# Optimization experiments

Measured on AMD Instinct MI355X. Metric: run time of the kernel, lower is better.

Reference implementation:

```python
import jax, jax.numpy as jnp
import numpy as np

D_MODEL, HEAD, B, S = 1024, 64, 4, 2048

def setup_inputs() -> dict:
    key = jax.random.key(0)
    ks = jax.random.split(key, 7)
    sc = 0.02
    return {
        "x": jax.random.normal(ks[0], (B, S, D_MODEL), dtype=jnp.float32),
        "w_q": jax.random.normal(ks[1], (D_MODEL, HEAD), dtype=jnp.float32) * sc,
        "b_q": jax.random.normal(ks[2], (HEAD,), dtype=jnp.float32) * sc,
        "w_k": jax.random.normal(ks[3], (D_MODEL, HEAD), dtype=jnp.float32) * sc,
        "b_k": jax.random.normal(ks[4], (HEAD,), dtype=jnp.float32) * sc,
        "w_v": jax.random.normal(ks[5], (D_MODEL, HEAD), dtype=jnp.float32) * sc,
        "b_v": jax.random.normal(ks[6], (HEAD,), dtype=jnp.float32) * sc,
    }

def reference(x, w_q, b_q, w_k, b_k, w_v, b_v):
    # q, k, v: [B, S, H]
    q = jnp.einsum('bsd,dh->bsh', x, w_q) + b_q
    k = jnp.einsum('bsd,dh->bsh', x, w_k) + b_k
    v = jnp.einsum('bsd,dh->bsh', x, w_v) + b_v
    head = k.shape[-1]
    # Source divides by (1/sqrt(d)) i.e. multiplies by sqrt(d) -- kept faithful.
    scores = jnp.einsum('bqh,bkh->bqk', q, k) * jnp.sqrt(jnp.float32(head))
    seq = x.shape[1]
    causal = jnp.tril(jnp.ones((seq, seq), dtype=bool))  # [S, S]
    scores = jnp.where(causal, scores, -jnp.inf)
    att = jax.nn.softmax(scores, axis=-1)
    # dropout is identity in eval / p=0
    return jnp.einsum('bqk,bkh->bqh', att, v)
```

## Files before the change

### kernel.cpp

```cpp
#include <hip/hip_runtime.h>
#include <math.h>

#define D_MODEL 1024
#define HEAD 64
#define BATCH 4
#define SEQ 2048
#define M_TOT (BATCH*SEQ)

typedef short short8 __attribute__((ext_vector_type(8)));
typedef float f32x4 __attribute__((ext_vector_type(4)));
typedef unsigned short ushort_t;

__device__ __forceinline__ unsigned short f2bf(float x) {
    union { float f; unsigned u; } v; v.f = x;
    unsigned r = (v.u + 0x7FFFu + ((v.u >> 16) & 1u)) >> 16;
    return (unsigned short)r;
}
__device__ __forceinline__ unsigned short f2bf_trunc(float x) {
    union { float f; unsigned u; } v; v.f = x;
    return (unsigned short)(v.u >> 16);
}
__device__ __forceinline__ float bf2f(unsigned short h) {
    union { unsigned u; float f; } v; v.u = ((unsigned)h) << 16;
    return v.f;
}

__global__ __launch_bounds__(256) void wsplit_kernel(
    const float* __restrict__ wq, const float* __restrict__ wk,
    const float* __restrict__ wv,
    ushort_t* __restrict__ Wfhi, ushort_t* __restrict__ Wflo)
{
    int tid = blockIdx.x * 256 + threadIdx.x;
    int l = tid & 63;
    int c = l & 15, g = l >> 4;
    int rest = tid >> 6;
    int nt = rest % 12, ks = rest / 12;
    const float* W = (nt < 4) ? wq : ((nt < 8) ? wk : wv);
    int colm = ((nt & 3) * 16) + c;
    short8 hi, lo;
#pragma unroll
    for (int e = 0; e < 8; ++e) {
        float v = W[(size_t)(32 * ks + 8 * g + e) * HEAD + colm];
        unsigned short h = f2bf_trunc(v);
        hi[e] = (short)h;
        lo[e] = (short)f2bf(v - bf2f(h));
    }
    *(short8*)&Wfhi[(size_t)tid * 8] = hi;
    *(short8*)&Wflo[(size_t)tid * 8] = lo;
}

__global__ __launch_bounds__(256) void proj_kernel(
    const float* __restrict__ x,
    const ushort_t* __restrict__ Wfhi, const ushort_t* __restrict__ Wflo,
    const float* __restrict__ bq, const float* __restrict__ bk,
    const float* __restrict__ bv,
    ushort_t* __restrict__ Qhi, ushort_t* __restrict__ Qlo,
    ushort_t* __restrict__ Khi, ushort_t* __restrict__ Klo,
    ushort_t* __restrict__ Vt)
{
    __shared__ float ld[4][16][33];
    const int t = threadIdx.x;
    const int w = t >> 6;
    const int l = t & 63;
    const int c = l & 15, g = l >> 4;
    const int job = blockIdx.x * 4 + w;
    const int mt = job / 6;
    const int ntg = job - mt * 6;
    const int m0 = mt * 16;

    f32x4 acc0 = (f32x4)0.0f, acc1 = (f32x4)0.0f;

    const float* xrow = &x[(size_t)(m0 + c) * D_MODEL + 8 * g];
    const size_t wbase = (size_t)(ntg * 2) * 512 + (size_t)l * 8;

#pragma unroll 4
    for (int ks = 0; ks < 32; ++ks) {
        const float* xp = xrow + 32 * ks;
        float4 a = *(const float4*)xp;
        float4 b2 = *(const float4*)(xp + 4);
        float xs[8] = {a.x, a.y, a.z, a.w, b2.x, b2.y, b2.z, b2.w};
        short8 xh, xl;
#pragma unroll
        for (int e = 0; e < 8; ++e) {
            unsigned short h = f2bf_trunc(xs[e]);
            xh[e] = (short)h;
            xl[e] = (short)f2bf(xs[e] - bf2f(h));
        }
        const size_t wo = wbase + (size_t)ks * 6144;
        short8 wh0 = *(const short8*)&Wfhi[wo];
        short8 wl0 = *(const short8*)&Wflo[wo];
        short8 wh1 = *(const short8*)&Wfhi[wo + 512];
        short8 wl1 = *(const short8*)&Wflo[wo + 512];
        acc0 = __builtin_amdgcn_mfma_f32_16x16x32_bf16(xh, wh0, acc0, 0, 0, 0);
        acc1 = __builtin_amdgcn_mfma_f32_16x16x32_bf16(xh, wh1, acc1, 0, 0, 0);
        acc0 = __builtin_amdgcn_mfma_f32_16x16x32_bf16(xl, wh0, acc0, 0, 0, 0);
        acc1 = __builtin_amdgcn_mfma_f32_16x16x32_bf16(xl, wh1, acc1, 0, 0, 0);
        acc0 = __builtin_amdgcn_mfma_f32_16x16x32_bf16(xh, wl0, acc0, 0, 0, 0);
        acc1 = __builtin_amdgcn_mfma_f32_16x16x32_bf16(xh, wl1, acc1, 0, 0, 0);
    }

#pragma unroll
    for (int r = 0; r < 4; ++r) {
        ld[w][4 * g + r][c] = acc0[r];
        ld[w][4 * g + r][16 + c] = acc1[r];
    }

    const int b = m0 >> 11;
    const int s0 = m0 & 2047;
    const int cb32 = (ntg & 1) * 32;

    if (ntg < 4) {
        const int row = l >> 2, cc = (l & 3) * 8;
        const float* bias = (ntg < 2) ? bq : bk;
        const float scale = (ntg < 2) ? 8.0f : 1.0f;
        ushort_t* Dhi = (ntg < 2) ? Qhi : Khi;
        ushort_t* Dlo = (ntg < 2) ? Qlo : Klo;
        short8 hi, lo;
#pragma unroll
        for (int i = 0; i < 8; ++i) {
            float v = (ld[w][row][cc + i] + bias[cb32 + cc + i]) * scale;
            unsigned short h = f2bf_trunc(v);
            hi[i] = (short)h;
            lo[i] = (short)f2bf(v - bf2f(h));
        }
        *(short8*)&Dhi[(size_t)(m0 + row) * HEAD + cb32 + cc] = hi;
        *(short8*)&Dlo[(size_t)(m0 + row) * HEAD + cb32 + cc] = lo;
    } else {
        const int dl = l >> 1, sh = (l & 1) * 8;
        const float bb = bv[cb32 + dl];
        short8 vv;
#pragma unroll
        for (int i = 0; i < 8; ++i)
            vv[i] = (short)f2bf(ld[w][sh + i][dl] + bb);
        *(short8*)&Vt[((size_t)b * HEAD + cb32 + dl) * SEQ + s0 + sh] = vv;
    }
}

#define NW 4
#define CHUNK 16

__global__ __launch_bounds__(256) void attn_kernel(
    const ushort_t* __restrict__ Qhi, const ushort_t* __restrict__ Qlo,
    const ushort_t* __restrict__ Khi, const ushort_t* __restrict__ Klo,
    const ushort_t* __restrict__ Vt, float* __restrict__ out)
{
    __shared__ float Po[NW][CHUNK][68];
    __shared__ float Pm[NW][CHUNK];
    __shared__ float Pl[NW][CHUNK];
    __shared__ __align__(16) ushort_t Plds[NW][CHUNK][72];

    const int t = threadIdx.x;
    const int w = t >> 6;
    const int l = t & 63;
    const int b = blockIdx.y;
    const int chunk = (int)gridDim.x - 1 - (int)blockIdx.x;
    const int q0 = chunk * CHUNK;
    const int c = l & 15;
    const int g = l >> 4;

    short8 qhi[2], qlo[2];
    {
        const ushort_t* qbase = &Qhi[(size_t)(b * SEQ + q0 + c) * HEAD];
        const ushort_t* qbasel = &Qlo[(size_t)(b * SEQ + q0 + c) * HEAD];
#pragma unroll
        for (int dc = 0; dc < 2; ++dc) {
            qhi[dc] = *(const short8*)&qbase[dc * 32 + 8 * g];
            qlo[dc] = *(const short8*)&qbasel[dc * 32 + 8 * g];
        }
    }

    f32x4 acc[4];
#pragma unroll
    for (int dt = 0; dt < 4; ++dt) acc[dt] = (f32x4)0.0f;
    float mrun = -1e30f, lsum = 0.f;

    const int ntiles = (q0 + CHUNK + 63) >> 6;
#pragma unroll 1
    for (int tile = w; tile < ntiles; tile += NW) {
        const int c0 = tile * 64;
        int nlive = ((q0 + 15 - c0) >> 4) + 1;
        nlive = nlive > 4 ? 4 : nlive;

        float sc[4][4];
        float pv[4][4];
#pragma unroll
        for (int t4 = 0; t4 < 4; ++t4)
#pragma unroll
            for (int r = 0; r < 4; ++r) pv[t4][r] = 0.f;

        float tmax = -1e30f;
#pragma unroll
        for (int t4 = 0; t4 < 4; ++t4) {
            if (t4 < nlive) {
                f32x4 st = (f32x4)0.0f;
                const size_t krow = (size_t)(b * SEQ + c0 + 16 * t4 + c) * HEAD;
#pragma unroll
                for (int dc = 0; dc < 2; ++dc) {
                    short8 khi = *(const short8*)&Khi[krow + dc * 32 + 8 * g];
                    short8 klo = *(const short8*)&Klo[krow + dc * 32 + 8 * g];
                    st = __builtin_amdgcn_mfma_f32_16x16x32_bf16(khi, qhi[dc], st, 0, 0, 0);
                    st = __builtin_amdgcn_mfma_f32_16x16x32_bf16(khi, qlo[dc], st, 0, 0, 0);
                    st = __builtin_amdgcn_mfma_f32_16x16x32_bf16(klo, qhi[dc], st, 0, 0, 0);
                }
#pragma unroll
                for (int r = 0; r < 4; ++r) {
                    int kv = c0 + 16 * t4 + 4 * g + r;
                    float s = (kv <= q0 + c) ? st[r] : -1e30f;
                    sc[t4][r] = s;
                    tmax = fmaxf(tmax, s);
                }
            }
        }
        tmax = fmaxf(tmax, __shfl_xor(tmax, 16));
        tmax = fmaxf(tmax, __shfl_xor(tmax, 32));
        float newm = fmaxf(mrun, tmax);
        float corr = __expf(mrun - newm);
        mrun = newm;

        float psum = 0.f;
#pragma unroll
        for (int t4 = 0; t4 < 4; ++t4) {
            if (t4 < nlive) {
#pragma unroll
                for (int r = 0; r < 4; ++r) {
                    float pp = __expf(sc[t4][r] - newm);
                    pv[t4][r] = pp;
                    psum += pp;
                }
            }
        }
        psum += __shfl_xor(psum, 16);
        psum += __shfl_xor(psum, 32);
        lsum = lsum * corr + psum;

#pragma unroll
        for (int r = 0; r < 4; ++r) {
            float cq = __shfl(corr, 4 * g + r);
#pragma unroll
            for (int dt = 0; dt < 4; ++dt) acc[dt][r] *= cq;
        }

#pragma unroll
        for (int t4 = 0; t4 < 4; ++t4) {
            uint2 u;
            u.x = (unsigned)f2bf(pv[t4][0]) | ((unsigned)f2bf(pv[t4][1]) << 16);
            u.y = (unsigned)f2bf(pv[t4][2]) | ((unsigned)f2bf(pv[t4][3]) << 16);
            *(uint2*)&Plds[w][c][16 * t4 + 4 * g] = u;
        }

        const int nkvc = (nlive + 1) >> 1;
#pragma unroll
        for (int kvc = 0; kvc < 2; ++kvc) {
            if (kvc < nkvc) {
                short8 pf = *(short8*)&Plds[w][c][kvc * 32 + 8 * g];
#pragma unroll
                for (int dt = 0; dt < 4; ++dt) {
                    const ushort_t* vp =
                        &Vt[((size_t)(b * HEAD) + 16 * dt + c) * SEQ + c0 + kvc * 32 + 8 * g];
                    short8 vf = *(const short8*)vp;
                    acc[dt] = __builtin_amdgcn_mfma_f32_16x16x32_bf16(pf, vf, acc[dt], 0, 0, 0);
                }
            }
        }
    }

    if (g == 0) { Pm[w][c] = mrun; Pl[w][c] = lsum; }
#pragma unroll
    for (int dt = 0; dt < 4; ++dt)
#pragma unroll
        for (int r = 0; r < 4; ++r)
            Po[w][4 * g + r][16 * dt + c] = acc[dt][r];
    __syncthreads();

    const int mr = t >> 4;
    const int md = (t & 15) * 4;
    float M = Pm[0][mr];
#pragma unroll
    for (int ww = 1; ww < NW; ++ww) M = fmaxf(M, Pm[ww][mr]);
    float L = 0.f;
    float4 O; O.x = O.y = O.z = O.w = 0.f;
#pragma unroll
    for (int ww = 0; ww < NW; ++ww) {
        float f = __expf(Pm[ww][mr] - M);
        L += f * Pl[ww][mr];
        float4 p = *(const float4*)&Po[ww][mr][md];
        O.x += f * p.x; O.y += f * p.y; O.z += f * p.z; O.w += f * p.w;
    }
    float inv = 1.0f / L;
    float4 res; res.x = O.x * inv; res.y = O.y * inv; res.z = O.z * inv; res.w = O.w * inv;
    *(float4*)&out[(size_t)(b * SEQ + q0 + mr) * HEAD + md] = res;
}

extern "C" void kernel_launch(void* const* d_in, const int* in_sizes, int n_in,
                              void* d_out, int out_size, void* d_ws, size_t ws_size,
                              hipStream_t stream) {
    (void)in_sizes; (void)n_in; (void)out_size; (void)ws_size;
    const float* x  = (const float*)d_in[0];
    const float* wq = (const float*)d_in[1];
    const float* bq = (const float*)d_in[2];
    const float* wk = (const float*)d_in[3];
    const float* bk = (const float*)d_in[4];
    const float* wv = (const float*)d_in[5];
    const float* bv = (const float*)d_in[6];
    float* out = (float*)d_out;

    ushort_t* Wfhi = (ushort_t*)d_ws;
    ushort_t* Wflo = Wfhi + (size_t)D_MODEL * 192;
    ushort_t* Qhi  = Wflo + (size_t)D_MODEL * 192;
    ushort_t* Qlo  = Qhi + (size_t)M_TOT * HEAD;
    ushort_t* Khi  = Qlo + (size_t)M_TOT * HEAD;
    ushort_t* Klo  = Khi + (size_t)M_TOT * HEAD;
    ushort_t* Vt   = Klo + (size_t)M_TOT * HEAD;

    hipLaunchKernelGGL(wsplit_kernel, dim3(96), dim3(256), 0, stream,
                       wq, wk, wv, Wfhi, Wflo);
    hipLaunchKernelGGL(proj_kernel, dim3(M_TOT / 16 * 6 / 4), dim3(256), 0, stream,
                       x, Wfhi, Wflo, bq, bk, bv, Qhi, Qlo, Khi, Klo, Vt);
    hipLaunchKernelGGL(attn_kernel, dim3(SEQ / CHUNK, BATCH), dim3(256), 0, stream,
                       Qhi, Qlo, Khi, Klo, Vt, out);
}
```

Baseline: 91.27 us.

## Split projection into 16-column jobs and use 8 waves per attention block

```diff
diff --git a/kernel.cpp b/kernel.cpp
--- a/kernel.cpp
+++ b/kernel.cpp
@@ -58,20 +58,19 @@
     ushort_t* __restrict__ Khi, ushort_t* __restrict__ Klo,
     ushort_t* __restrict__ Vt)
 {
-    __shared__ float ld[4][16][33];
+    __shared__ float ld[4][16][17];
     const int t = threadIdx.x;
     const int w = t >> 6;
     const int l = t & 63;
     const int c = l & 15, g = l >> 4;
     const int job = blockIdx.x * 4 + w;
-    const int mt = job / 6;
-    const int ntg = job - mt * 6;
+    const int mt = job / 12;
+    const int nt = job - mt * 12;
     const int m0 = mt * 16;
 
-    f32x4 acc0 = (f32x4)0.0f, acc1 = (f32x4)0.0f;
-
+    f32x4 acc = (f32x4)0.0f;
     const float* xrow = &x[(size_t)(m0 + c) * D_MODEL + 8 * g];
-    const size_t wbase = (size_t)(ntg * 2) * 512 + (size_t)l * 8;
+    const size_t wlane = (size_t)(nt * 64 + l) * 8;
 
 #pragma unroll 4
     for (int ks = 0; ks < 32; ++ks) {
@@ -86,60 +85,58 @@
             xh[e] = (short)h;
             xl[e] = (short)f2bf(xs[e] - bf2f(h));
         }
-        const size_t wo = wbase + (size_t)ks * 6144;
-        short8 wh0 = *(const short8*)&Wfhi[wo];
-        short8 wl0 = *(const short8*)&Wflo[wo];
-        short8 wh1 = *(const short8*)&Wfhi[wo + 512];
-        short8 wl1 = *(const short8*)&Wflo[wo + 512];
-        acc0 = __builtin_amdgcn_mfma_f32_16x16x32_bf16(xh, wh0, acc0, 0, 0, 0);
-        acc1 = __builtin_amdgcn_mfma_f32_16x16x32_bf16(xh, wh1, acc1, 0, 0, 0);
-        acc0 = __builtin_amdgcn_mfma_f32_16x16x32_bf16(xl, wh0, acc0, 0, 0, 0);
-        acc1 = __builtin_amdgcn_mfma_f32_16x16x32_bf16(xl, wh1, acc1, 0, 0, 0);
-        acc0 = __builtin_amdgcn_mfma_f32_16x16x32_bf16(xh, wl0, acc0, 0, 0, 0);
-        acc1 = __builtin_amdgcn_mfma_f32_16x16x32_bf16(xh, wl1, acc1, 0, 0, 0);
-    }
-
-#pragma unroll
-    for (int r = 0; r < 4; ++r) {
-        ld[w][4 * g + r][c] = acc0[r];
-        ld[w][4 * g + r][16 + c] = acc1[r];
-    }
+        const size_t wo = wlane + (size_t)ks * 6144;
+        short8 wh = *(const short8*)&Wfhi[wo];
+        short8 wl_ = *(const short8*)&Wflo[wo];
+        acc = __builtin_amdgcn_mfma_f32_16x16x32_bf16(xh, wh, acc, 0, 0, 0);
+        acc = __builtin_amdgcn_mfma_f32_16x16x32_bf16(xl, wh, acc, 0, 0, 0);
+        acc = __builtin_amdgcn_mfma_f32_16x16x32_bf16(xh, wl_, acc, 0, 0, 0);
+    }
+
+#pragma unroll
+    for (int r = 0; r < 4; ++r) ld[w][4 * g + r][c] = acc[r];
 
     const int b = m0 >> 11;
     const int s0 = m0 & 2047;
-    const int cb32 = (ntg & 1) * 32;
-
-    if (ntg < 4) {
-        const int row = l >> 2, cc = (l & 3) * 8;
-        const float* bias = (ntg < 2) ? bq : bk;
-        const float scale = (ntg < 2) ? 8.0f : 1.0f;
-        ushort_t* Dhi = (ntg < 2) ? Qhi : Khi;
-        ushort_t* Dlo = (ntg < 2) ? Qlo : Klo;
-        short8 hi, lo;
-#pragma unroll
-        for (int i = 0; i < 8; ++i) {
-            float v = (ld[w][row][cc + i] + bias[cb32 + cc + i]) * scale;
+    const int col16 = (nt & 3) * 16;
+
+    if (nt < 8) {
+        const int row = l >> 2, cc4 = (l & 3) * 4;
+        const float* bias = (nt < 4) ? bq : bk;
+        const float scale = (nt < 4) ? 8.0f : 1.0f;
+        ushort_t* Dhi = (nt < 4) ? Qhi : Khi;
+        ushort_t* Dlo = (nt < 4) ? Qlo : Klo;
+        unsigned hu[2] = {0, 0}, lu[2] = {0, 0};
+#pragma unroll
+        for (int i = 0; i < 4; ++i) {
+            float v = (ld[w][row][cc4 + i] + bias[col16 + cc4 + i]) * scale;
             unsigned short h = f2bf_trunc(v);
-            hi[i] = (short)h;
-            lo[i] = (short)f2bf(v - bf2f(h));
-        }
-        *(short8*)&Dhi[(size_t)(m0 + row) * HEAD + cb32 + cc] = hi;
-        *(short8*)&Dlo[(size_t)(m0 + row) * HEAD + cb32 + cc] = lo;
+            unsigned short lo = f2bf(v - bf2f(h));
+            hu[i >> 1] |= ((unsigned)h) << ((i & 1) * 16);
+            lu[i >> 1] |= ((unsigned)lo) << ((i & 1) * 16);
+        }
+        size_t off = (size_t)(m0 + row) * HEAD + col16 + cc4;
+        *(uint2*)&Dhi[off] = make_uint2(hu[0], hu[1]);
+        *(uint2*)&Dlo[off] = make_uint2(lu[0], lu[1]);
     } else {
-        const int dl = l >> 1, sh = (l & 1) * 8;
-        const float bb = bv[cb32 + dl];
-        short8 vv;
-#pragma unroll
-        for (int i = 0; i < 8; ++i)
-            vv[i] = (short)f2bf(ld[w][sh + i][dl] + bb);
-        *(short8*)&Vt[((size_t)b * HEAD + cb32 + dl) * SEQ + s0 + sh] = vv;
-    }
-}
-
-#define NW 4
+        const int dl = l >> 2, sg = (l & 3) * 4;
+        const float bb = bv[col16 + dl];
+        unsigned vu[2] = {0, 0};
+#pragma unroll
+        for (int i = 0; i < 4; ++i) {
+            unsigned short v = f2bf(ld[w][sg + i][dl] + bb);
+            vu[i >> 1] |= ((unsigned)v) << ((i & 1) * 16);
+        }
+        *(uint2*)&Vt[((size_t)b * HEAD + col16 + dl) * SEQ + s0 + sg] =
+            make_uint2(vu[0], vu[1]);
+    }
+}
+
+#define NW 8
 #define CHUNK 16
-
-__global__ __launch_bounds__(256) void attn_kernel(
+#define PSTR 88
+
+__global__ __launch_bounds__(512) void attn_kernel(
     const ushort_t* __restrict__ Qhi, const ushort_t* __restrict__ Qlo,
     const ushort_t* __restrict__ Khi, const ushort_t* __restrict__ Klo,
     const ushort_t* __restrict__ Vt, float* __restrict__ out)
@@ -147,7 +144,7 @@
     __shared__ float Po[NW][CHUNK][68];
     __shared__ float Pm[NW][CHUNK];
     __shared__ float Pl[NW][CHUNK];
-    __shared__ __align__(16) ushort_t Plds[NW][CHUNK][72];
+    __shared__ __align__(16) ushort_t Plds[NW][CHUNK][PSTR];
 
     const int t = threadIdx.x;
     const int w = t >> 6;
@@ -272,23 +269,25 @@
             Po[w][4 * g + r][16 * dt + c] = acc[dt][r];
     __syncthreads();
 
-    const int mr = t >> 4;
-    const int md = (t & 15) * 4;
-    float M = Pm[0][mr];
-#pragma unroll
-    for (int ww = 1; ww < NW; ++ww) M = fmaxf(M, Pm[ww][mr]);
-    float L = 0.f;
-    float4 O; O.x = O.y = O.z = O.w = 0.f;
-#pragma unroll
-    for (int ww = 0; ww < NW; ++ww) {
-        float f = __expf(Pm[ww][mr] - M);
-        L += f * Pl[ww][mr];
-        float4 p = *(const float4*)&Po[ww][mr][md];
-        O.x += f * p.x; O.y += f * p.y; O.z += f * p.z; O.w += f * p.w;
-    }
-    float inv = 1.0f / L;
-    float4 res; res.x = O.x * inv; res.y = O.y * inv; res.z = O.z * inv; res.w = O.w * inv;
-    *(float4*)&out[(size_t)(b * SEQ + q0 + mr) * HEAD + md] = res;
+    if (t < 256) {
+        const int mr = t >> 4;
+        const int md = (t & 15) * 4;
+        float M = Pm[0][mr];
+#pragma unroll
+        for (int ww = 1; ww < NW; ++ww) M = fmaxf(M, Pm[ww][mr]);
+        float L = 0.f;
+        float4 O; O.x = O.y = O.z = O.w = 0.f;
+#pragma unroll
+        for (int ww = 0; ww < NW; ++ww) {
+            float f = __expf(Pm[ww][mr] - M);
+            L += f * Pl[ww][mr];
+            float4 p = *(const float4*)&Po[ww][mr][md];
+            O.x += f * p.x; O.y += f * p.y; O.z += f * p.z; O.w += f * p.w;
+        }
+        float inv = 1.0f / L;
+        float4 res; res.x = O.x * inv; res.y = O.y * inv; res.z = O.z * inv; res.w = O.w * inv;
+        *(float4*)&out[(size_t)(b * SEQ + q0 + mr) * HEAD + md] = res;
+    }
 }
 
 extern "C" void kernel_launch(void* const* d_in, const int* in_sizes, int n_in,
@@ -314,8 +313,8 @@
 
     hipLaunchKernelGGL(wsplit_kernel, dim3(96), dim3(256), 0, stream,
                        wq, wk, wv, Wfhi, Wflo);
-    hipLaunchKernelGGL(proj_kernel, dim3(M_TOT / 16 * 6 / 4), dim3(256), 0, stream,
+    hipLaunchKernelGGL(proj_kernel, dim3(M_TOT / 16 * 12 / 4), dim3(256), 0, stream,
                        x, Wfhi, Wflo, bq, bk, bv, Qhi, Qlo, Khi, Klo, Vt);
-    hipLaunchKernelGGL(attn_kernel, dim3(SEQ / CHUNK, BATCH), dim3(256), 0, stream,
+    hipLaunchKernelGGL(attn_kernel, dim3(SEQ / CHUNK, BATCH), dim3(512), 0, stream,
                        Qhi, Qlo, Khi, Klo, Vt, out);
 }
```

Measured after the change: 112.3 us. +23.1%, slower.
